# Kernel tuning notes

Hardware: AMD Instinct MI355X
Metric: run time of the kernel (lower is better)

Reference implementation:

```python
import jax, jax.numpy as jnp
import numpy as np

S = 3        # num_scale
C = 256      # codebook / feature dim
K = 512      # codebook size


def _bilinear_down(x, f):
    # torch F.interpolate(scale_factor=1/f, mode='bilinear', align_corners=False)
    # for even integer f: src = (i+0.5)*f - 0.5 = f*i + (f//2 - 1) + 0.5 -> avg of 2 neighbors.
    o = f // 2 - 1
    x = (x[:, :, o::f, :] + x[:, :, o + 1::f, :]) * 0.5
    x = (x[:, :, :, o::f] + x[:, :, :, o + 1::f]) * 0.5
    return x


def _encode(img, w, b):
    # stride-4 patchify conv: (b,3,H,W) -> (b,C,H/4,W/4), NCHW
    y = jax.lax.conv_general_dilated(img, w, (4, 4), 'VALID',
                                     dimension_numbers=('NCHW', 'OIHW', 'NCHW'))
    return y + b[None, :, None, None]


def _match(e, cb):
    # e [..., c], cb [K, c]. logits = -||e - cb||^2; zsoft = softmax(logits).
    # Only max-prob and argmax are consumed downstream, so compute them stably.
    d = (jnp.sum(e * e, -1, keepdims=True)
         - 2.0 * jnp.einsum('...c,kc->...k', e, cb)
         + jnp.sum(cb * cb, -1))
    logits = -d
    zidx = jnp.argmax(logits, -1)
    maxprob = jnp.exp(jnp.max(logits, -1) - jax.scipy.special.logsumexp(logits, -1))
    return maxprob, zidx


def _resample(e, j, i):
    # e is NHWC at scale j; bring it to scale i (avg_pool if j<i, nearest upsample if j>i)
    if j == i:
        return e
    if j < i:
        f = 2 ** (i - j)
        b, h, w, c = e.shape
        return e.reshape(b, h // f, f, w // f, f, c).mean(axis=(2, 4))
    f = 2 ** (j - i)
    return jnp.repeat(jnp.repeat(e, f, axis=1), f, axis=2)


def setup_inputs() -> dict:
    key = jax.random.key(0)
    k1, k2, k3 = jax.random.split(key, 3)
    image = jax.random.normal(k1, (8, 3, 256, 256), jnp.float32)
    conv_w = jax.random.normal(k2, (C, 3, 4, 4), jnp.float32) * 0.05
    conv_b = jnp.zeros((C,), jnp.float32)
    codebooks = jax.random.normal(k3, (1 + S, K, C), jnp.float32) * 0.05
    return {"image": image, "conv_w": conv_w, "conv_b": conv_b, "codebooks": codebooks}


def reference(image, conv_w, conv_b, codebooks):
    # multi-scale inputs (bilinear downsample), shared encoder per scale
    imgs = [image] + [_bilinear_down(image, 2 ** k) for k in range(1, S)]
    encodes = [_encode(im, conv_w, conv_b) for im in imgs]          # NCHW, sizes 64/32/16
    enc_nhwc = [jnp.transpose(e, (0, 2, 3, 1)) for e in encodes]

    cb0 = codebooks[0]
    # ms_fuse, scale i1 = 0 (only scale 0 is returned when decode=None, retr=True):
    stack = jnp.stack([_resample(enc_nhwc[j], j, 0) for j in range(S)])  # [s,b,h,w,c]
    prob1, idx1 = _match(stack, cb0)                                      # [s,b,h,w]
    sel = jnp.argmax(prob1, 0)                                            # [b,h,w] best scale
    zidx1 = jnp.take_along_axis(idx1, sel[None], 0)[0]                    # [b,h,w]
    enc1 = jnp.take_along_axis(stack, sel[None, ..., None], 0)[0]         # [b,h,w,c]
    quant1 = cb0[zidx1]

    # per-scale quantizer for scale 0
    _, zidx2 = _match(enc_nhwc[0], codebooks[1])
    quant2 = codebooks[1][zidx2]

    zidx0 = jnp.stack([zidx1, zidx2], -1)            # [b,h,w,2]
    e_fused = (enc1 + enc_nhwc[0]) * 0.5
    q_fused = (quant1 + quant2) * 0.5
    # alpha = 0 -> residual == quant; naive STE
    ste0 = e_fused + jax.lax.stop_gradient(q_fused - e_fused)

    return (encodes[0],
            jnp.transpose(zidx0, (0, 3, 1, 2)),
            jnp.transpose(ste0, (0, 3, 1, 2)))
```

## Files before the change

### kernel.cpp

```cpp
#include <hip/hip_runtime.h>
#include <math.h>


#define FEAT12_OFF 0
#define FBLO_OFF   2621440
#define PART_OFF   11010048
#define PROB_OFF   13434880
#define IDX1_OFF   13477888
#define IDX2_OFF   13520896
#define CNF_OFF    13553664
#define CND_OFF    13554688
#define CBS_OFF    13556736
#define IMG1_OFF   13818880
#define IMG2_OFF   14212096
#define RLIST_OFF  14310400
#define DLIST_OFF  14386176
#define CNT_OFF    14418944

#define EPS_V 1e-3f
#define EPS_P_REL 2e-3f

typedef __attribute__((ext_vector_type(8))) short short8;
typedef __attribute__((ext_vector_type(4))) float f32x4;

__device__ inline unsigned short f2bf(float x) {
    unsigned u = __float_as_uint(x);
    return (unsigned short)((u + 0x7FFFu + ((u >> 16) & 1u)) >> 16);
}
__device__ inline float bf2f(unsigned short h) {
    return __uint_as_float(((unsigned)h) << 16);
}
__device__ inline int rswz(int row) { return (row & 3) ^ ((row >> 2) & 3); }

__device__ inline void glds16(const unsigned short* g, unsigned short* l) {
    __builtin_amdgcn_global_load_lds(
        (const __attribute__((address_space(1))) void*)g,
        (__attribute__((address_space(3))) void*)l, 16, 0, 0);
}

__device__ inline float feat_elem(const float* __restrict__ out0,
                                  const float* __restrict__ feat12,
                                  int fr, int c) {
    if (fr < 32768) {
        int b = fr >> 12, y = (fr >> 6) & 63, x = fr & 63;
        return out0[(((size_t)b * 256 + c) * 64 + y) * 64 + x];
    }
    return feat12[(size_t)(fr - 32768) * 256 + c];
}

__launch_bounds__(256)
__global__ void prep(const float* __restrict__ image,
                     const float* __restrict__ codebooks,
                     float* __restrict__ img1, float* __restrict__ img2,
                     double* __restrict__ cnd, float* __restrict__ cnf,
                     unsigned short* __restrict__ cbs, int* __restrict__ cnt) {
    int bid = blockIdx.x, tid = threadIdx.x;
    if (bid == 0 && tid < 2) cnt[tid] = 0;
    if (bid < 1536) {
        int i = bid * 256 + tid;
        int x = i & 127;
        int t = i >> 7;
        int y = t & 127;
        int bc = t >> 7;
        const float* base = image + ((size_t)bc * 256 + (size_t)(y * 2)) * 256;
        int cx = x * 2;
        float v00 = base[cx],     v10 = base[256 + cx];
        float v01 = base[cx + 1], v11 = base[256 + cx + 1];
        img1[i] = ((v00 + v10) * 0.5f + (v01 + v11) * 0.5f) * 0.5f;
    } else if (bid < 1920) {
        int i = (bid - 1536) * 256 + tid;
        int x = i & 63;
        int t = i >> 6;
        int y = t & 63;
        int bc = t >> 6;
        const float* base = image + ((size_t)bc * 256 + (size_t)(y * 4 + 1)) * 256;
        int cx = x * 4 + 1;
        float v00 = base[cx],     v10 = base[256 + cx];
        float v01 = base[cx + 1], v11 = base[256 + cx + 1];
        img2[i] = ((v00 + v10) * 0.5f + (v01 + v11) * 0.5f) * 0.5f;
    } else if (bid < 2176) {
        int row = (bid - 1920) * 4 + (tid >> 6);
        int lane = tid & 63;
        const float* p = codebooks + (size_t)row * 256;
        double s = 0.0;
        for (int c = lane; c < 256; c += 64) {
            double v = (double)p[c];
            s = fma(v, v, s);
        }
        #pragma unroll
        for (int off = 32; off; off >>= 1) s += __shfl_down(s, off);
        if (lane == 0) { cnd[row] = s; cnf[row] = (float)s; }
    } else {
        int i = (bid - 2176) * 256 + tid;
        int book = i >> 17, rem = i & 131071;
        int code = rem >> 8, ch = rem & 255;
        float c = codebooks[(size_t)book * 131072 + rem];
        unsigned short h0 = f2bf(c);
        unsigned short h1 = f2bf(c - bf2f(h0));
        int codeblk = code >> 7, row = code & 127;
        int kc = ch >> 5, q = (ch >> 3) & 3, j = ch & 7;
        int qs = q ^ rswz(row);
        size_t off = ((((size_t)(book * 2) * 4 + codeblk) * 8 + kc) * 128 + row) * 32 + qs * 8 + j;
        cbs[off] = h0;
        cbs[off + 4 * 32768] = h1;
    }
}

__launch_bounds__(256)
__global__ void encode_all(const float* __restrict__ image,
                           const float* __restrict__ img1,
                           const float* __restrict__ img2,
                           const float* __restrict__ w,
                           const float* __restrict__ bias,
                           float* __restrict__ feat12,
                           unsigned short* __restrict__ fbh,
                           unsigned short* __restrict__ fbl,
                           float* __restrict__ out0) {
    __shared__ float patch[12 * 128];
    __shared__ __align__(16) unsigned short pk[2][8][2][256];
    __shared__ __align__(16) float vf[2][8][256];
    int bid = blockIdx.x;
    const float* img; int Hout, rowbase, local, xbase, npos, Wimg, WL, colbase;
    int isS0 = 0;
    if (bid < 1024) {
        img = image; Hout = 64; rowbase = 0; isS0 = 1;
        local = bid >> 1; int half = bid & 1;
        xbase = half * 32; npos = 32; Wimg = 256; WL = 128; colbase = half * 128;
    } else if (bid < 1280) {
        img = img1; Hout = 32; rowbase = 32768;
        local = bid - 1024; xbase = 0; npos = 32; Wimg = 128; WL = 128; colbase = 0;
    } else {
        img = img2; Hout = 16; rowbase = 40960;
        local = bid - 1280; xbase = 0; npos = 16; Wimg = 64; WL = 64; colbase = 0;
    }
    int Wout = Hout;
    int tid = threadIdx.x;
    int b = local / Hout, y = local % Hout;
    int Himg = Hout * 4;

    const float* ibase = img + (size_t)b * 3 * Himg * Wimg;
    int nload = 12 * WL;
    for (int i = tid; i < nload; i += 256) {
        int cl = i % WL, r = i / WL;
        int ci = r >> 2, kh = r & 3;
        patch[r * WL + cl] = ibase[((size_t)ci * Himg + 4 * y + kh) * Wimg + colbase + cl];
    }
    float wr[48];
    #pragma unroll
    for (int j = 0; j < 48; j++) wr[j] = w[tid * 48 + j];
    float bv = bias[tid];
    __syncthreads();

    int rb = rowbase + (b * Hout + y) * Wout + xbase;
    for (int x0 = 0; x0 < npos; x0 += 8) {
        int buf = (x0 >> 3) & 1;
        #pragma unroll
        for (int p = 0; p < 8; p++) {
            int xl = x0 + p;
            float acc = 0.f;
            #pragma unroll
            for (int ci = 0; ci < 3; ci++)
                #pragma unroll
                for (int kh = 0; kh < 4; kh++) {
                    const float* pr = &patch[(ci * 4 + kh) * WL + 4 * xl];
                    #pragma unroll
                    for (int kw = 0; kw < 4; kw++)
                        acc = fmaf(pr[kw], wr[ci * 16 + kh * 4 + kw], acc);
                }
            float val = acc + bv;
            unsigned short hi = f2bf(val);
            pk[buf][p][0][tid] = hi;
            pk[buf][p][1][tid] = f2bf(val - bf2f(hi));
            vf[buf][p][tid] = val;
            if (!isS0) feat12[(size_t)(rb + xl - 32768) * 256 + tid] = val;
        }
        __syncthreads();
        #pragma unroll
        for (int s = tid; s < 512; s += 256) {
            int fp = s >> 6; int rest = s & 63;
            int fwp = rest >> 5, fkc = (rest >> 2) & 7, fwg = rest & 3;
            int r = rb + x0 + fp;
            int rowblk = r >> 7, rrow = r & 127;
            int ch0 = fkc * 32 + ((fwg ^ rswz(rrow)) << 3);
            uint4 v = *(const uint4*)&pk[buf][fp][fwp][ch0];
            size_t off = (((size_t)rowblk * 8 + fkc) * 128 + rrow) * 32 + fwg * 8;
            if (fwp) *(uint4*)&fbl[off] = v;
            else     *(uint4*)&fbh[off] = v;
        }
        if (isS0) {
            int c = tid;
            size_t o = (((size_t)b * 256 + c) * 64 + y) * 64 + (xbase + x0);
            float4 v0 = make_float4(vf[buf][0][c], vf[buf][1][c], vf[buf][2][c], vf[buf][3][c]);
            float4 v1 = make_float4(vf[buf][4][c], vf[buf][5][c], vf[buf][6][c], vf[buf][7][c]);
            *(float4*)&out0[o]     = v0;
            *(float4*)&out0[o + 4] = v1;
        }
    }
}

__launch_bounds__(256, 2)
__global__ void match_bulk(const unsigned short* __restrict__ fbh,
                           const unsigned short* __restrict__ fbl,
                           const unsigned short* __restrict__ cbs,
                           const float* __restrict__ cnf,
                           float* __restrict__ partials) {
    __shared__ unsigned short A0s[2][4096], A1s[2][4096], B0s[2][4096], B1s[2][4096];
    int bid0 = blockIdx.x;
    int bid = (bid0 & 7) * 296 + (bid0 >> 3);
    int codeblk = bid & 3, rowtile = bid >> 2;
    int book = (rowtile >= 336) ? 1 : 0;
    int rowblk = book ? rowtile - 336 : rowtile;
    int vr0 = rowtile * 128;
    int tid = threadIdx.x;
    int wid = tid >> 6, l = tid & 63;
    int waveY = wid & 1, waveX = wid >> 1;
    int lm = l & 15, lq = l >> 4;
    int slot = lq ^ rswz(lm);
    int wlds = wid * 512;

    f32x4 acc[4][4];
    #pragma unroll
    for (int ct = 0; ct < 4; ct++)
        #pragma unroll
        for (int rt = 0; rt < 4; rt++) acc[ct][rt] = (f32x4)0.0f;

    const unsigned short* gA0 = fbh + (size_t)rowblk * 32768 + tid * 8;
    const unsigned short* gA1 = fbl + (size_t)rowblk * 32768 + tid * 8;
    const unsigned short* gB0 = cbs + ((size_t)(book * 8) + codeblk) * 32768 + tid * 8;
    const unsigned short* gB1 = gB0 + 4 * 32768;

    auto STAGE = [&](int buf, int kc) {
        const unsigned short* ga0 = gA0 + kc * 4096;
        const unsigned short* ga1 = gA1 + kc * 4096;
        const unsigned short* gb0 = gB0 + kc * 4096;
        const unsigned short* gb1 = gB1 + kc * 4096;
        #pragma unroll
        for (int i = 0; i < 2; i++) {
            glds16(ga0 + i * 2048, &A0s[buf][i * 2048 + wlds]);
            glds16(ga1 + i * 2048, &A1s[buf][i * 2048 + wlds]);
            glds16(gb0 + i * 2048, &B0s[buf][i * 2048 + wlds]);
            glds16(gb1 + i * 2048, &B1s[buf][i * 2048 + wlds]);
        }
    };

    short8 a0[4], a1[4], b0[4], b1[4];
    auto LOADFRAG = [&](int cur) {
        #pragma unroll
        for (int t = 0; t < 4; t++) {
            int ra = (waveY * 64 + t * 16 + lm) * 32 + slot * 8;
            int rbx = (waveX * 64 + t * 16 + lm) * 32 + slot * 8;
            a0[t] = *(const short8*)&A0s[cur][ra];
            a1[t] = *(const short8*)&A1s[cur][ra];
            b0[t] = *(const short8*)&B0s[cur][rbx];
            b1[t] = *(const short8*)&B1s[cur][rbx];
        }
    };
    auto DOMFMA = [&]() {
        __builtin_amdgcn_s_setprio(1);
        #pragma unroll
        for (int ct = 0; ct < 4; ct++)
            #pragma unroll
            for (int rt = 0; rt < 4; rt++) {
                acc[ct][rt] = __builtin_amdgcn_mfma_f32_16x16x32_bf16(b0[ct], a0[rt], acc[ct][rt], 0, 0, 0);
                acc[ct][rt] = __builtin_amdgcn_mfma_f32_16x16x32_bf16(b1[ct], a0[rt], acc[ct][rt], 0, 0, 0);
                acc[ct][rt] = __builtin_amdgcn_mfma_f32_16x16x32_bf16(b0[ct], a1[rt], acc[ct][rt], 0, 0, 0);
            }
        __builtin_amdgcn_s_setprio(0);
    };

    STAGE(0, 0);
    STAGE(1, 1);

#define MB_STEP(KC)                                                        \
    do {                                                                   \
        asm volatile("s_waitcnt vmcnt(8)" ::: "memory");                   \
        __builtin_amdgcn_s_barrier();                                      \
        __builtin_amdgcn_sched_barrier(0);                                 \
        LOADFRAG((KC) & 1);                                                \
        asm volatile("s_waitcnt lgkmcnt(0)" ::: "memory");                 \
        __builtin_amdgcn_sched_barrier(0);                                 \
        __builtin_amdgcn_s_barrier();                                      \
        __builtin_amdgcn_sched_barrier(0);                                 \
        STAGE((KC) & 1, (KC) + 2);                                         \
        DOMFMA();                                                          \
    } while (0)

    MB_STEP(0); MB_STEP(1); MB_STEP(2); MB_STEP(3); MB_STEP(4); MB_STEP(5);
#undef MB_STEP

    asm volatile("s_waitcnt vmcnt(8)" ::: "memory");
    __builtin_amdgcn_s_barrier();
    __builtin_amdgcn_sched_barrier(0);
    LOADFRAG(0);
    asm volatile("s_waitcnt lgkmcnt(0)" ::: "memory");
    __builtin_amdgcn_sched_barrier(0);
    DOMFMA();
    asm volatile("s_waitcnt vmcnt(0)" ::: "memory");
    __builtin_amdgcn_s_barrier();
    __builtin_amdgcn_sched_barrier(0);
    LOADFRAG(1);
    asm volatile("s_waitcnt lgkmcnt(0)" ::: "memory");
    __builtin_amdgcn_sched_barrier(0);
    DOMFMA();

    int kbase = codeblk * 128 + waveX * 64 + lq * 4;
    float4 cnv4[4];
    #pragma unroll
    for (int ct = 0; ct < 4; ct++)
        cnv4[ct] = *(const float4*)&cnf[book * 512 + kbase + ct * 16];
    float4* part4 = (float4*)partials;

    #pragma unroll
    for (int rt = 0; rt < 4; rt++) {
        float v[4][4];
        #pragma unroll
        for (int ct = 0; ct < 4; ct++) {
            v[ct][0] = 2.0f * acc[ct][rt][0] - cnv4[ct].x;
            v[ct][1] = 2.0f * acc[ct][rt][1] - cnv4[ct].y;
            v[ct][2] = 2.0f * acc[ct][rt][2] - cnv4[ct].z;
            v[ct][3] = 2.0f * acc[ct][rt][3] - cnv4[ct].w;
        }
        float m1 = v[0][0], m2 = -3.4e38f;
        int k1 = kbase;
        #pragma unroll
        for (int ct = 0; ct < 4; ct++)
            #pragma unroll
            for (int j = 0; j < 4; j++) {
                if (ct == 0 && j == 0) continue;
                float val = v[ct][j];
                if (val > m1) { m2 = m1; m1 = val; k1 = kbase + ct * 16 + j; }
                else m2 = fmaxf(m2, val);
            }
        #pragma unroll
        for (int off = 16; off < 64; off <<= 1) {
            float mo1 = __shfl_xor(m1, off);
            float mo2 = __shfl_xor(m2, off);
            int ko1 = __shfl_xor(k1, off);
            if (mo1 > m1 || (mo1 == m1 && ko1 < k1)) { m2 = fmaxf(m1, mo2); m1 = mo1; k1 = ko1; }
            else m2 = fmaxf(m2, mo1);
        }
        float s = 0.f;
        if (!book) {
            #pragma unroll
            for (int ct = 0; ct < 4; ct++)
                #pragma unroll
                for (int j = 0; j < 4; j++) s += __expf(v[ct][j] - m1);
            #pragma unroll
            for (int off = 16; off < 64; off <<= 1) s += __shfl_xor(s, off);
        }
        if (lq == 0) {
            int vr = vr0 + waveY * 64 + rt * 16 + lm;
            float4 st = make_float4(m1, m2, __int_as_float(k1), s);
            part4[(size_t)vr * 8 + codeblk * 2 + waveX] = st;
        }
    }
}

__global__ void combine_rows(const float* __restrict__ partials,
                             int* __restrict__ idx1, int* __restrict__ idx2,
                             float* __restrict__ prob,
                             int* __restrict__ rlist, int* __restrict__ cnt) {
    int vr = blockIdx.x * 256 + threadIdx.x;
    const float4* p = (const float4*)partials + (size_t)vr * 8;
    float sm[8], ss[8];
    float4 a = p[0];
    float m1 = a.x, m2 = a.y; int k1 = __float_as_int(a.z);
    sm[0] = a.x; ss[0] = a.w;
    #pragma unroll
    for (int j = 1; j < 8; j++) {
        float4 b = p[j];
        sm[j] = b.x; ss[j] = b.w;
        int kk = __float_as_int(b.z);
        if (b.x > m1 || (b.x == m1 && kk < k1)) { m2 = fmaxf(m1, b.y); m1 = b.x; k1 = kk; }
        else m2 = fmaxf(m2, b.x);
    }
    float S = 0.f;
    #pragma unroll
    for (int j = 0; j < 8; j++) S += ss[j] * __expf(sm[j] - m1);
    if (vr < 43008) { idx1[vr] = k1; prob[vr] = 1.0f / S; }
    else idx2[vr - 43008] = k1;
    if (m1 - m2 < EPS_V) { int pos = atomicAdd(cnt, 1); rlist[pos] = vr; }
}

__launch_bounds__(256)
__global__ void rescue_exact(const float* __restrict__ out0,
                             const float* __restrict__ feat12,
                             const float* __restrict__ codebooks,
                             const double* __restrict__ cnd,
                             const int* __restrict__ rlist, const int* __restrict__ cnt,
                             int* __restrict__ idx1, int* __restrict__ idx2,
                             float* __restrict__ prob) {
    __shared__ double sfd[256];
    __shared__ double rv[4]; __shared__ int rk[4]; __shared__ double rs[4];
    __shared__ double gvmax; __shared__ int gkmax;
    int tid = threadIdx.x;
    int lane = tid & 63, wave = tid >> 6;
    int n = cnt[0];
    for (int e = blockIdx.x; e < n; e += gridDim.x) {
        int vr = rlist[e];
        int book = vr >= 43008;
        int fr = book ? vr - 43008 : vr;
        sfd[tid] = (double)feat_elem(out0, feat12, fr, tid);
        __syncthreads();
        const float* cb = codebooks + (size_t)book * 131072;
        double vloc[2]; int kk[2];
        #pragma unroll
        for (int h = 0; h < 2; h++) {
            int k = h * 256 + tid;
            const float* cp = cb + (size_t)k * 256;
            double d0 = 0.0, d1 = 0.0, d2 = 0.0, d3 = 0.0;
            for (int c = 0; c < 256; c += 4) {
                float4 cv = *(const float4*)&cp[c];
                d0 = fma((double)cv.x, sfd[c],     d0);
                d1 = fma((double)cv.y, sfd[c + 1], d1);
                d2 = fma((double)cv.z, sfd[c + 2], d2);
                d3 = fma((double)cv.w, sfd[c + 3], d3);
            }
            double dot = (d0 + d1) + (d2 + d3);
            vloc[h] = 2.0 * dot - cnd[book * 512 + k];
            kk[h] = k;
        }
        double bv = vloc[0]; int bk = kk[0];
        if (vloc[1] > bv || (vloc[1] == bv && kk[1] < bk)) { bv = vloc[1]; bk = kk[1]; }
        #pragma unroll
        for (int off = 32; off; off >>= 1) {
            double vo = __shfl_xor(bv, off);
            int ko = __shfl_xor(bk, off);
            if (vo > bv || (vo == bv && ko < bk)) { bv = vo; bk = ko; }
        }
        if (lane == 0) { rv[wave] = bv; rk[wave] = bk; }
        __syncthreads();
        if (tid == 0) {
            double v0 = rv[0]; int K = rk[0];
            #pragma unroll
            for (int w = 1; w < 4; w++)
                if (rv[w] > v0 || (rv[w] == v0 && rk[w] < K)) { v0 = rv[w]; K = rk[w]; }
            gvmax = v0; gkmax = K;
        }
        __syncthreads();
        double vm = gvmax;
        double s = exp(vloc[0] - vm) + exp(vloc[1] - vm);
        #pragma unroll
        for (int off = 32; off; off >>= 1) s += __shfl_xor(s, off);
        if (lane == 0) rs[wave] = s;
        __syncthreads();
        if (tid == 0) {
            double S = ((rs[0] + rs[1]) + rs[2]) + rs[3];
            if (book) idx2[fr] = gkmax;
            else { idx1[vr] = gkmax; prob[vr] = (float)(1.0 / S); }
        }
        __syncthreads();
    }
}

__launch_bounds__(256)
__global__ void fuse1(const float* __restrict__ prob,
                      const int* __restrict__ idx1, const int* __restrict__ idx2,
                      const float* __restrict__ codebooks,
                      float* __restrict__ outZ, float* __restrict__ outS,
                      int* __restrict__ dlist, int* __restrict__ cnt) {
    __shared__ int i1_s[64], i2_s[64], defer_s[64];
    int tid = threadIdx.x;
    int bid = blockIdx.x;
    int chh = bid & 1;
    int rowid = bid >> 1;
    int b = rowid >> 6, y = rowid & 63;

    if (tid < 64) {
        int x = tid;
        int r0 = (b * 64 + y) * 64 + x;
        int r1 = 32768 + (b * 32 + (y >> 1)) * 32 + (x >> 1);
        int r2 = 40960 + (b * 16 + (y >> 2)) * 16 + (x >> 2);
        float p0 = prob[r0], p1 = prob[r1], p2 = prob[r2];
        int rsel = r0; float best = p0;
        if (p1 > best) { best = p1; rsel = r1; }
        if (p2 > best) { best = p2; rsel = r2; }
        float second = (rsel == r0) ? fmaxf(p1, p2)
                     : (rsel == r1) ? fmaxf(p0, p2) : fmaxf(p0, p1);
        int defer = (best - second < EPS_P_REL * best) ? 1 : 0;
        defer_s[x] = defer;
        if (defer) {
            if (chh == 0) {
                int pos = atomicAdd(cnt + 1, 1);
                dlist[pos] = (b << 12) | (y << 6) | x;
            }
            i1_s[x] = 0; i2_s[x] = 0;
        } else {
            int i1 = idx1[rsel], i2 = idx2[r0];
            i1_s[x] = i1; i2_s[x] = i2;
            if (chh == 0) {
                size_t zb = (size_t)b * 8192 + (size_t)y * 64 + x;
                outZ[zb] = (float)i1;
                outZ[zb + 4096] = (float)i2;
            }
        }
    }
    __syncthreads();

    int x = tid & 63, cc = tid >> 6;
    const float* q1p = codebooks + (size_t)i1_s[x] * 256;
    const float* q2p = codebooks + (size_t)(512 + i2_s[x]) * 256;
    if (defer_s[x]) return;
    #pragma unroll
    for (int it = 0; it < 8; it++) {
        int c = chh * 128 + it * 16 + cc * 4;
        float4 q1 = *(const float4*)&q1p[c];
        float4 q2 = *(const float4*)&q2p[c];
        size_t o = (((size_t)b * 256 + c) * 64 + y) * 64 + x;
        outS[o]         = (q1.x + q2.x) * 0.5f;
        outS[o + 4096]  = (q1.y + q2.y) * 0.5f;
        outS[o + 8192]  = (q1.z + q2.z) * 0.5f;
        outS[o + 12288] = (q1.w + q2.w) * 0.5f;
    }
}

__launch_bounds__(256)
__global__ void fuse2(const float* __restrict__ out0,
                      const float* __restrict__ feat12,
                      const float* __restrict__ codebooks,
                      const double* __restrict__ cnd,
                      const int* __restrict__ idx2,
                      const int* __restrict__ dlist, const int* __restrict__ cnt,
                      float* __restrict__ outZ, float* __restrict__ outS) {
    __shared__ double sfd[256];
    __shared__ double rv[4]; __shared__ int rk[4]; __shared__ double rs[4];
    __shared__ double gvmax;
    __shared__ double pRes[3]; __shared__ int kRes[3];
    __shared__ int selS, i2S;
    int tid = threadIdx.x;
    int lane = tid & 63, wave = tid >> 6;
    int n = cnt[1];
    for (int e = blockIdx.x; e < n; e += gridDim.x) {
        int px = dlist[e];
        int b = px >> 12, y = (px >> 6) & 63, x = px & 63;
        int r0 = (b * 64 + y) * 64 + x;
        int r1 = 32768 + (b * 32 + (y >> 1)) * 32 + (x >> 1);
        int r2 = 40960 + (b * 16 + (y >> 2)) * 16 + (x >> 2);
        int rows[3] = {r0, r1, r2};
        for (int s3 = 0; s3 < 3; s3++) {
            sfd[tid] = (double)feat_elem(out0, feat12, rows[s3], tid);
            __syncthreads();
            double vloc[2];
            #pragma unroll
            for (int h = 0; h < 2; h++) {
                int k = h * 256 + tid;
                const float* cp = codebooks + (size_t)k * 256;
                double d0 = 0.0, d1 = 0.0, d2 = 0.0, d3 = 0.0;
                for (int c = 0; c < 256; c += 4) {
                    float4 cv = *(const float4*)&cp[c];
                    d0 = fma((double)cv.x, sfd[c],     d0);
                    d1 = fma((double)cv.y, sfd[c + 1], d1);
                    d2 = fma((double)cv.z, sfd[c + 2], d2);
                    d3 = fma((double)cv.w, sfd[c + 3], d3);
                }
                double dot = (d0 + d1) + (d2 + d3);
                vloc[h] = 2.0 * dot - cnd[k];
            }
            double bv = vloc[0]; int bk = tid;
            if (vloc[1] > bv) { bv = vloc[1]; bk = tid + 256; }
            #pragma unroll
            for (int off = 32; off; off >>= 1) {
                double vo = __shfl_xor(bv, off);
                int ko = __shfl_xor(bk, off);
                if (vo > bv || (vo == bv && ko < bk)) { bv = vo; bk = ko; }
            }
            if (lane == 0) { rv[wave] = bv; rk[wave] = bk; }
            __syncthreads();
            if (tid == 0) {
                double v0 = rv[0]; int K = rk[0];
                #pragma unroll
                for (int w = 1; w < 4; w++)
                    if (rv[w] > v0 || (rv[w] == v0 && rk[w] < K)) { v0 = rv[w]; K = rk[w]; }
                gvmax = v0; kRes[s3] = K;
            }
            __syncthreads();
            double vm = gvmax;
            double s = exp(vloc[0] - vm) + exp(vloc[1] - vm);
            #pragma unroll
            for (int off = 32; off; off >>= 1) s += __shfl_xor(s, off);
            if (lane == 0) rs[wave] = s;
            __syncthreads();
            if (tid == 0) pRes[s3] = 1.0 / (((rs[0] + rs[1]) + rs[2]) + rs[3]);
            __syncthreads();
        }
        if (tid == 0) {
            int sel = 0; double best = pRes[0];
            if (pRes[1] > best) { best = pRes[1]; sel = 1; }
            if (pRes[2] > best) { best = pRes[2]; sel = 2; }
            selS = sel;
            int i2 = idx2[r0];
            i2S = i2;
            size_t zb = (size_t)b * 8192 + (size_t)y * 64 + x;
            outZ[zb] = (float)kRes[sel];
            outZ[zb + 4096] = (float)i2;
        }
        __syncthreads();
        int sel = selS;
        int c = tid;
        float q1 = codebooks[(size_t)kRes[sel] * 256 + c];
        float q2 = codebooks[(size_t)(512 + i2S) * 256 + c];
        size_t o = (((size_t)b * 256 + c) * 64 + y) * 64 + x;
        outS[o] = (q1 + q2) * 0.5f;
        __syncthreads();
    }
}

extern "C" void kernel_launch(void* const* d_in, const int* in_sizes, int n_in,
                              void* d_out, int out_size, void* d_ws, size_t ws_size,
                              hipStream_t stream) {
    (void)in_sizes; (void)n_in; (void)out_size; (void)ws_size;
    const float* image     = (const float*)d_in[0];
    const float* conv_w    = (const float*)d_in[1];
    const float* conv_b    = (const float*)d_in[2];
    const float* codebooks = (const float*)d_in[3];

    float*  ws     = (float*)d_ws;
    float*  feat12 = ws + FEAT12_OFF;
    unsigned short* fbl = (unsigned short*)(ws + FBLO_OFF);
    float*  parts  = ws + PART_OFF;
    float*  prob   = ws + PROB_OFF;
    int*    idx1   = (int*)(ws + IDX1_OFF);
    int*    idx2   = (int*)(ws + IDX2_OFF);
    float*  cnf    = ws + CNF_OFF;
    double* cnd    = (double*)(ws + CND_OFF);
    unsigned short* cbs = (unsigned short*)(ws + CBS_OFF);
    float*  img1   = ws + IMG1_OFF;
    float*  img2   = ws + IMG2_OFF;
    int*    rlist  = (int*)(ws + RLIST_OFF);
    int*    dlist  = (int*)(ws + DLIST_OFF);
    int*    cnt    = (int*)(ws + CNT_OFF);

    float* out  = (float*)d_out;
    float* out0 = out;
    float* outZ = out + 8388608;
    float* outS = out + 8454144;
    unsigned short* fbh = (unsigned short*)outS;

    prep<<<3200, 256, 0, stream>>>(image, codebooks, img1, img2, cnd, cnf, cbs, cnt);
    encode_all<<<1408, 256, 0, stream>>>(image, img1, img2, conv_w, conv_b,
                                         feat12, fbh, fbl, out0);
    match_bulk<<<2368, 256, 0, stream>>>(fbh, fbl, cbs, cnf, parts);
    combine_rows<<<296, 256, 0, stream>>>(parts, idx1, idx2, prob, rlist, cnt);
    rescue_exact<<<1024, 256, 0, stream>>>(out0, feat12, codebooks, cnd, rlist, cnt,
                                           idx1, idx2, prob);
    fuse1<<<1024, 256, 0, stream>>>(prob, idx1, idx2, codebooks, outZ, outS, dlist, cnt);
    fuse2<<<512, 256, 0, stream>>>(out0, feat12, codebooks, cnd, idx2, dlist, cnt,
                                   outZ, outS);
}
```

Measured before the change: 277.9 us.

## Relocate workspace buffers into output and stage combine partials through LDS

```diff
diff --git a/kernel.cpp b/kernel.cpp
--- a/kernel.cpp
+++ b/kernel.cpp
@@ -2,20 +2,17 @@
 #include <math.h>
 
 
-#define FEAT12_OFF 0
-#define FBLO_OFF   2621440
-#define PART_OFF   11010048
-#define PROB_OFF   13434880
-#define IDX1_OFF   13477888
-#define IDX2_OFF   13520896
-#define CNF_OFF    13553664
-#define CND_OFF    13554688
-#define CBS_OFF    13556736
-#define IMG1_OFF   13818880
-#define IMG2_OFF   14212096
-#define RLIST_OFF  14310400
-#define DLIST_OFF  14386176
-#define CNT_OFF    14418944
+#define FEAT12_OFF 11010048
+#define PROB_OFF   13631488
+#define IDX1_OFF   13674496
+#define IDX2_OFF   13717504
+#define CNF_OFF    13750272
+#define CND_OFF    13751296
+#define CBS_OFF    13753344
+#define DLIST_OFF  14015488
+#define CNT_OFF    14048256
+
+#define PLANE_STRIDE 11010048
 
 #define EPS_V 1e-3f
 #define EPS_P_REL 2e-3f
@@ -113,8 +110,7 @@
                            const float* __restrict__ w,
                            const float* __restrict__ bias,
                            float* __restrict__ feat12,
-                           unsigned short* __restrict__ fbh,
-                           unsigned short* __restrict__ fbl,
+                           unsigned short* __restrict__ featbf,
                            float* __restrict__ out0) {
     __shared__ float patch[12 * 128];
     __shared__ __align__(16) unsigned short pk[2][8][2][256];
@@ -183,9 +179,9 @@
             int rowblk = r >> 7, rrow = r & 127;
             int ch0 = fkc * 32 + ((fwg ^ rswz(rrow)) << 3);
             uint4 v = *(const uint4*)&pk[buf][fp][fwp][ch0];
-            size_t off = (((size_t)rowblk * 8 + fkc) * 128 + rrow) * 32 + fwg * 8;
-            if (fwp) *(uint4*)&fbl[off] = v;
-            else     *(uint4*)&fbh[off] = v;
+            size_t off = (((size_t)rowblk * 8 + fkc) * 128 + rrow) * 32 + fwg * 8
+                       + (size_t)fwp * PLANE_STRIDE;
+            *(uint4*)&featbf[off] = v;
         }
         if (isS0) {
             int c = tid;
@@ -199,8 +195,7 @@
 }
 
 __launch_bounds__(256, 2)
-__global__ void match_bulk(const unsigned short* __restrict__ fbh,
-                           const unsigned short* __restrict__ fbl,
+__global__ void match_bulk(const unsigned short* __restrict__ featbf,
                            const unsigned short* __restrict__ cbs,
                            const float* __restrict__ cnf,
                            float* __restrict__ partials) {
@@ -224,8 +219,8 @@
         #pragma unroll
         for (int rt = 0; rt < 4; rt++) acc[ct][rt] = (f32x4)0.0f;
 
-    const unsigned short* gA0 = fbh + (size_t)rowblk * 32768 + tid * 8;
-    const unsigned short* gA1 = fbl + (size_t)rowblk * 32768 + tid * 8;
+    const unsigned short* gA0 = featbf + (size_t)rowblk * 32768 + tid * 8;
+    const unsigned short* gA1 = gA0 + PLANE_STRIDE;
     const unsigned short* gB0 = cbs + ((size_t)(book * 8) + codeblk) * 32768 + tid * 8;
     const unsigned short* gB1 = gB0 + 4 * 32768;
 
@@ -356,19 +351,29 @@
     }
 }
 
+__launch_bounds__(256)
 __global__ void combine_rows(const float* __restrict__ partials,
                              int* __restrict__ idx1, int* __restrict__ idx2,
                              float* __restrict__ prob,
                              int* __restrict__ rlist, int* __restrict__ cnt) {
-    int vr = blockIdx.x * 256 + threadIdx.x;
-    const float4* p = (const float4*)partials + (size_t)vr * 8;
+    __shared__ __align__(16) float4 tile[256][9];
+    int tid = threadIdx.x;
+    const float4* p4 = (const float4*)partials;
+    size_t base = (size_t)blockIdx.x * 2048;
+    #pragma unroll
+    for (int k = 0; k < 8; k++) {
+        int j = k * 256 + tid;
+        tile[j >> 3][j & 7] = p4[base + j];
+    }
+    __syncthreads();
+    int vr = blockIdx.x * 256 + tid;
     float sm[8], ss[8];
-    float4 a = p[0];
+    float4 a = tile[tid][0];
     float m1 = a.x, m2 = a.y; int k1 = __float_as_int(a.z);
     sm[0] = a.x; ss[0] = a.w;
     #pragma unroll
     for (int j = 1; j < 8; j++) {
-        float4 b = p[j];
+        float4 b = tile[tid][j];
         sm[j] = b.x; ss[j] = b.w;
         int kk = __float_as_int(b.z);
         if (b.x > m1 || (b.x == m1 && kk < k1)) { m2 = fmaxf(m1, b.y); m1 = b.x; k1 = kk; }
@@ -615,18 +620,14 @@
     const float* codebooks = (const float*)d_in[3];
 
     float*  ws     = (float*)d_ws;
+    unsigned short* featbf = (unsigned short*)ws;
     float*  feat12 = ws + FEAT12_OFF;
-    unsigned short* fbl = (unsigned short*)(ws + FBLO_OFF);
-    float*  parts  = ws + PART_OFF;
     float*  prob   = ws + PROB_OFF;
     int*    idx1   = (int*)(ws + IDX1_OFF);
     int*    idx2   = (int*)(ws + IDX2_OFF);
     float*  cnf    = ws + CNF_OFF;
     double* cnd    = (double*)(ws + CND_OFF);
     unsigned short* cbs = (unsigned short*)(ws + CBS_OFF);
-    float*  img1   = ws + IMG1_OFF;
-    float*  img2   = ws + IMG2_OFF;
-    int*    rlist  = (int*)(ws + RLIST_OFF);
     int*    dlist  = (int*)(ws + DLIST_OFF);
     int*    cnt    = (int*)(ws + CNT_OFF);
 
@@ -634,12 +635,15 @@
     float* out0 = out;
     float* outZ = out + 8388608;
     float* outS = out + 8454144;
-    unsigned short* fbh = (unsigned short*)outS;
+    float* img1  = out + 8388608;
+    float* img2  = out + 8781824;
+    float* parts = out + 8880128;
+    int*   rlist = (int*)(out + 11304960);
 
     prep<<<3200, 256, 0, stream>>>(image, codebooks, img1, img2, cnd, cnf, cbs, cnt);
     encode_all<<<1408, 256, 0, stream>>>(image, img1, img2, conv_w, conv_b,
-                                         feat12, fbh, fbl, out0);
-    match_bulk<<<2368, 256, 0, stream>>>(fbh, fbl, cbs, cnf, parts);
+                                         feat12, featbf, out0);
+    match_bulk<<<2368, 256, 0, stream>>>(featbf, cbs, cnf, parts);
     combine_rows<<<296, 256, 0, stream>>>(parts, idx1, idx2, prob, rlist, cnt);
     rescue_exact<<<1024, 256, 0, stream>>>(out0, feat12, codebooks, cnd, rlist, cnt,
                                            idx1, idx2, prob);
```

Result: slower. 291.2 us (+4.8%).
